# Kernel tuning notes

Measured on AMD Instinct MI355X. Metric: run time of the kernel, lower is better.

Reference implementation:

```python
import jax, jax.numpy as jnp
import numpy as np

CHUNK = (10, 10, 10)          # chunk_shape from init_kwargs
VSHAPE = (40, 40, 200)        # spatial shape of each block
GRID_MAX = 1000               # locations drawn from [0, GRID_MAX)
SPAN = 256                    # > (GRID_MAX + max(VSHAPE)) / min(CHUNK); per-dim chunk-grid span for key linearization
NBATCH = 64


def setup_inputs() -> dict:
    key = jax.random.key(0)
    k1, k2 = jax.random.split(key)
    data = jax.random.normal(k1, (NBATCH, *VSHAPE), dtype=jnp.float32)
    location = jax.random.randint(k2, (NBATCH, 3), 0, GRID_MAX, dtype=jnp.int32)
    return {"data": data, "location": location}


def _chunkify(data, location):
    """Rebin each block into chunk-grid-aligned tiles of shape CHUNK.
    data: [B, V0, V1, V2]; location: [B, 3] int offsets in the global grid.
    Returns (chunks [M, *CHUNK], locs [M, 3]) with M = B * prod(nchunks)."""
    B = data.shape[0]
    C = jnp.array(CHUNK, dtype=jnp.int32)
    shift = location % C          # [B,3] offset of block origin within its first chunk
    start = location - shift      # [B,3] chunk-aligned envelope origin
    # Fixed-size envelope V + C per dim covers any shift in [0, C).
    E = tuple(v + c for v, c in zip(VSHAPE, CHUNK))
    nch = tuple(e // c for e, c in zip(E, CHUNK))  # chunks per dim: (5, 5, 21)

    def pad_one(d, sh):
        # padded[j0,j1,j2] = d[j - sh] where in range, else 0 (gather + mask, no scatter)
        idx = [jnp.arange(E[k]) - sh[k] for k in range(3)]
        valid = [(ix >= 0) & (ix < VSHAPE[k]) for k, ix in enumerate(idx)]
        cidx = [jnp.clip(ix, 0, VSHAPE[k] - 1) for k, ix in enumerate(idx)]
        g = d[cidx[0][:, None, None], cidx[1][None, :, None], cidx[2][None, None, :]]
        m = valid[0][:, None, None] & valid[1][None, :, None] & valid[2][None, None, :]
        return jnp.where(m, g, jnp.float32(0))

    padded = jax.vmap(pad_one)(data, shift)  # [B, E0, E1, E2]
    padded = padded.reshape(B, nch[0], CHUNK[0], nch[1], CHUNK[1], nch[2], CHUNK[2])
    chunks = padded.transpose(0, 1, 3, 5, 2, 4, 6).reshape(-1, *CHUNK)
    # per-chunk global locations
    g = jnp.stack(jnp.meshgrid(jnp.arange(nch[0]), jnp.arange(nch[1]),
                               jnp.arange(nch[2]), indexing='ij'), axis=-1)  # [n0,n1,n2,3]
    locs = start[:, None, None, None, :] + g[None].astype(jnp.int32) * C     # [B,n0,n1,n2,3]
    return chunks, locs.reshape(-1, 3)


def _accumulate(chunks, locs):
    """Sum chunks sharing the same global chunk location (scatter-add reduce).
    Output padded to a fixed M rows (jit-friendly); padding rows are zero."""
    M = chunks.shape[0]
    C = jnp.array(CHUNK, dtype=jnp.int32)
    cg = locs // C  # chunk-grid coordinates, each < SPAN
    keys = (cg[:, 0] * SPAN + cg[:, 1]) * SPAN + cg[:, 2]  # int32 linearized key
    ukeys, inv = jnp.unique(keys, return_inverse=True, size=M,
                            fill_value=jnp.int32(2**31 - 1))
    out = jax.ops.segment_sum(chunks.reshape(M, -1), inv, num_segments=M)
    out = out.reshape(M, *CHUNK)
    uloc = jnp.stack([ukeys // (SPAN * SPAN), (ukeys // SPAN) % SPAN,
                      ukeys % SPAN], axis=-1).astype(jnp.int32) * C
    return out, uloc


def reference(data, location):
    chunks, locs = _chunkify(data, location)
    return _accumulate(chunks, locs)
```

## Files before the change

### kernel.cpp

```cpp
#include <hip/hip_runtime.h>
#include <hip/hip_bf16.h>

namespace {
constexpr int NB    = 64;
constexpr int V0d   = 40, V1d = 40, V2d = 200;
constexpr int VOL   = V0d * V1d * V2d;
constexpr int NC0   = 5, NC1 = 5, NC2 = 21;
constexpr int CELLS = NC0 * NC1 * NC2;
constexpr int M     = NB * CELLS;
constexpr int C1MAX = 104, C2MAX = 120;
constexpr int KS    = 104 * C1MAX * C2MAX;
constexpr int SEG   = 4096;
constexpr int NSEG  = (KS + SEG - 1) / SEG;
constexpr int KSP   = NSEG * SEG;
constexpr int CHVOL = 1000;
}

__device__ __forceinline__ float bf16r(float v) {
    return __bfloat162float(__float2bfloat16(v));
}

__device__ __forceinline__ int enc(int c0, int c1, int c2) {
    return (c0 * C1MAX + c1) * C2MAX + c2;
}

__global__ void k_zero(int* __restrict__ P, int4* __restrict__ mask4) {
    int idx = blockIdx.x * blockDim.x + threadIdx.x;
    int stride = gridDim.x * blockDim.x;
    int4* p4 = reinterpret_cast<int4*>(P);
    const int n4 = KSP / 4;
    for (int i = idx; i < n4; i += stride) p4[i] = make_int4(0, 0, 0, 0);
    const int m4 = M * 8 / 16;
    for (int i = idx; i < m4; i += stride) mask4[i] = make_int4(0, 0, 0, 0);
}

__global__ void k_mark(const int* __restrict__ loc, int* __restrict__ P) {
    int m = blockIdx.x * blockDim.x + threadIdx.x;
    if (m >= M) return;
    int b = m / CELLS, cell = m % CELLS;
    int i = cell / (NC1 * NC2), j = (cell / NC2) % NC1, k = cell % NC2;
    P[enc(loc[b * 3 + 0] / 10 + i, loc[b * 3 + 1] / 10 + j,
          loc[b * 3 + 2] / 10 + k)] = 1;
}

__global__ __launch_bounds__(256) void k_scan_blocks(int* __restrict__ P,
                                                     int* __restrict__ Bsums) {
    int bid = blockIdx.x, t = threadIdx.x;
    int4* p4 = reinterpret_cast<int4*>(P + (size_t)bid * SEG + t * 16);
    int4 a = p4[0], b = p4[1], c = p4[2], d = p4[3];
    int v[16] = {a.x, a.y, a.z, a.w, b.x, b.y, b.z, b.w,
                 c.x, c.y, c.z, c.w, d.x, d.y, d.z, d.w};
    int s = 0;
#pragma unroll
    for (int e = 0; e < 16; ++e) s += v[e];
    __shared__ int sc[256];
    sc[t] = s;
    __syncthreads();
#pragma unroll
    for (int off = 1; off < 256; off <<= 1) {
        int x = (t >= off) ? sc[t - off] : 0;
        __syncthreads();
        sc[t] += x;
        __syncthreads();
    }
    int incl = sc[t];
    if (t == 255) Bsums[bid] = incl;
    int run = incl - s;
#pragma unroll
    for (int e = 0; e < 16; ++e) { int x = v[e]; v[e] = run; run += x; }
    p4[0] = make_int4(v[0], v[1], v[2], v[3]);
    p4[1] = make_int4(v[4], v[5], v[6], v[7]);
    p4[2] = make_int4(v[8], v[9], v[10], v[11]);
    p4[3] = make_int4(v[12], v[13], v[14], v[15]);
}

__global__ __launch_bounds__(256) void k_scan_sums(int* __restrict__ Bsums,
                                                   int* __restrict__ U) {
    __shared__ int sc[256];
    __shared__ int carry_s;
    int t = threadIdx.x;
    if (t == 0) carry_s = 0;
    __syncthreads();
    for (int base = 0; base < NSEG; base += 256) {
        int idx = base + t;
        int vv = (idx < NSEG) ? Bsums[idx] : 0;
        sc[t] = vv;
        __syncthreads();
#pragma unroll
        for (int off = 1; off < 256; off <<= 1) {
            int x = (t >= off) ? sc[t - off] : 0;
            __syncthreads();
            sc[t] += x;
            __syncthreads();
        }
        int incl = sc[t];
        int carry = carry_s;
        if (idx < NSEG) Bsums[idx] = carry + incl - vv;
        __syncthreads();
        if (t == 255) carry_s = carry + incl;
        __syncthreads();
    }
    if (t == 0) U[0] = carry_s;
}

__global__ void k_slots(const int* __restrict__ loc, const int* __restrict__ P,
                        const int* __restrict__ Bsums, int* __restrict__ ukeys,
                        unsigned long long* __restrict__ mask) {
    int m = blockIdx.x * blockDim.x + threadIdx.x;
    if (m >= M) return;
    int b = m / CELLS, cell = m % CELLS;
    int i = cell / (NC1 * NC2), j = (cell / NC2) % NC1, k = cell % NC2;
    int d = enc(loc[b * 3 + 0] / 10 + i, loc[b * 3 + 1] / 10 + j,
                loc[b * 3 + 2] / 10 + k);
    int rank = P[d] + Bsums[d / SEG];
    ukeys[rank] = d;
    atomicOr(&mask[rank], 1ull << b);
}

__global__ __launch_bounds__(256) void k_out(const float* __restrict__ data,
                                             const int* __restrict__ loc,
                                             const int* __restrict__ ukeys,
                                             const unsigned long long* __restrict__ mask,
                                             const int* __restrict__ U,
                                             float* __restrict__ out,
                                             long long base_ul) {
    int orig = blockIdx.x;
    int r = (orig & 7) * (M / 8) + (orig >> 3);
    int t = threadIdx.x;

    __shared__ int sloc[NB * 3];
    __shared__ int skey, sU;
    __shared__ unsigned long long smask;
    if (t < NB * 3) sloc[t] = loc[t];
    if (t == 0) {
        sU = U[0];
        skey = ukeys[r];
        smask = mask[r];
    }
    __syncthreads();

    bool valid = (r < sU);
    float acc[4] = {0.f, 0.f, 0.f, 0.f};
    int c0 = 0, c1 = 0, c2 = 0;
    if (valid) {
        int d = skey;
        c0 = d / (C1MAX * C2MAX);
        int rem = d % (C1MAX * C2MAX);
        c1 = rem / C2MAX;
        c2 = rem % C2MAX;
        int g0 = c0 * 10, g1 = c1 * 10, g2 = c2 * 10;
        int ex[4], ey[4], ez[4];
#pragma unroll
        for (int q = 0; q < 4; ++q) {
            int e = t + 256 * q;
            ex[q] = e / 100; ey[q] = (e / 10) % 10; ez[q] = e % 10;
        }
        unsigned long long mk = smask;
        while (mk) {
            int b = __builtin_ctzll(mk);
            mk &= mk - 1;
            int l0 = sloc[b * 3 + 0], l1 = sloc[b * 3 + 1], l2 = sloc[b * 3 + 2];
            const float* db = data + (size_t)b * VOL;
            int o0 = g0 - l0, o1 = g1 - l1, o2 = g2 - l2;
#pragma unroll
            for (int q = 0; q < 4; ++q) {
                int e = t + 256 * q;
                if (e < CHVOL) {
                    int p0 = o0 + ex[q], p1 = o1 + ey[q], p2 = o2 + ez[q];
                    if ((unsigned)p0 < (unsigned)V0d &&
                        (unsigned)p1 < (unsigned)V1d &&
                        (unsigned)p2 < (unsigned)V2d)
                        acc[q] += db[(p0 * V1d + p1) * V2d + p2];
                }
            }
        }
    }
#pragma unroll
    for (int q = 0; q < 4; ++q) {
        int e = t + 256 * q;
        if (e < CHVOL)
            out[(long long)r * CHVOL + e] = bf16r(acc[q]);
    }
    if (t == 0) {
        float u0, u1, u2;
        if (valid) {
            u0 = (float)(c0 * 10);
            u1 = (float)(c1 * 10);
            u2 = (float)(c2 * 10);
        } else {
            u0 = 327670.f; u1 = 2550.f; u2 = 2550.f;
        }
        long long i = base_ul + (long long)r * 3;
        out[i + 0] = bf16r(u0);
        out[i + 1] = bf16r(u1);
        out[i + 2] = bf16r(u2);
    }
}

extern "C" void kernel_launch(void* const* d_in, const int* in_sizes, int n_in,
                              void* d_out, int out_size, void* d_ws, size_t ws_size,
                              hipStream_t stream) {
    const float* data = (const float*)d_in[0];
    const int* loc    = (const int*)d_in[1];
    float* out        = (float*)d_out;

    const size_t bytesP  = (size_t)KSP * 4;
    const size_t bytesSm = (size_t)M * 8
                         + (size_t)(NSEG + 64) * 4
                         + (size_t)M * 4 + 64;
    char* ws = (char*)d_ws;
    int* P;
    char* smalls;
    if (ws_size >= bytesP + bytesSm) {
        P      = (int*)ws;
        smalls = ws + bytesP;
    } else {
        P      = (int*)d_out;
        smalls = ws;
    }
    unsigned long long* mask = (unsigned long long*)smalls;
    int* Bsums = (int*)(smalls + (size_t)M * 8);
    int* ukeys = Bsums + NSEG + 64;
    int* U     = ukeys + M;

    long long out_sz  = (long long)out_size;
    long long base_ul = out_sz - (long long)3 * M;

    k_zero<<<640, 256, 0, stream>>>(P, (int4*)mask);
    k_mark<<<(M + 255) / 256, 256, 0, stream>>>(loc, P);
    k_scan_blocks<<<NSEG, 256, 0, stream>>>(P, Bsums);
    k_scan_sums<<<1, 256, 0, stream>>>(Bsums, U);
    k_slots<<<(M + 255) / 256, 256, 0, stream>>>(loc, P, Bsums, ukeys, mask);
    k_out<<<M, 256, 0, stream>>>(data, loc, ukeys, mask, U, out, base_ul);
}
```

Baseline: 70.69 us.

## Process four output chunks per block with branchless prefetched gathers and float4 stores

The output kernel now handles four unique chunk rows per block instead of one. Each thread owns four contiguous elements, which allows float4 stores. The first contributing source block for every row is loaded up front with clamped, predicated gathers so the loads can be issued together, and the shared-memory staging and barrier are removed. The trade-offs are more registers, four times fewer blocks, and serial per-row loops over any remaining contributors.

```diff
diff --git a/kernel.cpp b/kernel.cpp
--- a/kernel.cpp
+++ b/kernel.cpp
@@ -14,6 +14,8 @@
 constexpr int NSEG  = (KS + SEG - 1) / SEG;
 constexpr int KSP   = NSEG * SEG;
 constexpr int CHVOL = 1000;
+constexpr int RPB   = 4;
+constexpr int NQ    = M / RPB;
 }
 
 __device__ __forceinline__ float bf16r(float v) {
@@ -125,72 +127,104 @@
                                              float* __restrict__ out,
                                              long long base_ul) {
     int orig = blockIdx.x;
-    int r = (orig & 7) * (M / 8) + (orig >> 3);
+    int q = (orig & 7) * (NQ / 8) + (orig >> 3);
+    int r0 = q * RPB;
     int t = threadIdx.x;
-
-    __shared__ int sloc[NB * 3];
-    __shared__ int skey, sU;
-    __shared__ unsigned long long smask;
-    if (t < NB * 3) sloc[t] = loc[t];
-    if (t == 0) {
-        sU = U[0];
-        skey = ukeys[r];
-        smask = mask[r];
-    }
-    __syncthreads();
-
-    bool valid = (r < sU);
-    float acc[4] = {0.f, 0.f, 0.f, 0.f};
-    int c0 = 0, c1 = 0, c2 = 0;
-    if (valid) {
-        int d = skey;
-        c0 = d / (C1MAX * C2MAX);
+    int U0 = U[0];
+
+    int e0 = t * 4;
+    int xj[4], yj[4], zj[4];
+#pragma unroll
+    for (int j = 0; j < 4; ++j) {
+        int e = e0 + j;
+        xj[j] = e / 100; yj[j] = (e / 10) % 10; zj[j] = e % 10;
+    }
+
+    float acc[RPB][4] = {};
+    unsigned long long mk2[RPB];
+    int c0v[RPB], c1v[RPB], c2v[RPB];
+    bool vR[RPB];
+
+#pragma unroll
+    for (int rk = 0; rk < RPB; ++rk) {
+        int r = r0 + rk;
+        bool valid = (r < U0);
+        vR[rk] = valid;
+        int d = valid ? ukeys[r] : 0;
+        unsigned long long mk = valid ? mask[r] : 0ull;
+        int c0 = d / (C1MAX * C2MAX);
         int rem = d % (C1MAX * C2MAX);
-        c1 = rem / C2MAX;
-        c2 = rem % C2MAX;
-        int g0 = c0 * 10, g1 = c1 * 10, g2 = c2 * 10;
-        int ex[4], ey[4], ez[4];
-#pragma unroll
-        for (int q = 0; q < 4; ++q) {
-            int e = t + 256 * q;
-            ex[q] = e / 100; ey[q] = (e / 10) % 10; ez[q] = e % 10;
-        }
-        unsigned long long mk = smask;
+        int c1 = rem / C2MAX, c2 = rem % C2MAX;
+        c0v[rk] = c0; c1v[rk] = c1; c2v[rk] = c2;
+        bool any = (mk != 0ull);
+        int b = any ? __builtin_ctzll(mk) : 0;
+        mk2[rk] = any ? (mk & (mk - 1)) : 0ull;
+        int l0 = loc[b * 3 + 0], l1 = loc[b * 3 + 1], l2 = loc[b * 3 + 2];
+        int o0 = any ? (c0 * 10 - l0) : -1000;
+        int o1 = c1 * 10 - l1, o2 = c2 * 10 - l2;
+        const float* db = data + (size_t)b * VOL;
+#pragma unroll
+        for (int j = 0; j < 4; ++j) {
+            int p0 = o0 + xj[j], p1 = o1 + yj[j], p2 = o2 + zj[j];
+            bool v = ((unsigned)p0 < (unsigned)V0d) &
+                     ((unsigned)p1 < (unsigned)V1d) &
+                     ((unsigned)p2 < (unsigned)V2d);
+            int lin = (p0 * V1d + p1) * V2d + p2;
+            lin = lin < 0 ? 0 : (lin > VOL - 1 ? VOL - 1 : lin);
+            float val = db[lin];
+            acc[rk][j] += v ? val : 0.f;
+        }
+    }
+
+#pragma unroll
+    for (int rk = 0; rk < RPB; ++rk) {
+        unsigned long long mk = mk2[rk];
         while (mk) {
             int b = __builtin_ctzll(mk);
             mk &= mk - 1;
-            int l0 = sloc[b * 3 + 0], l1 = sloc[b * 3 + 1], l2 = sloc[b * 3 + 2];
+            int l0 = loc[b * 3 + 0], l1 = loc[b * 3 + 1], l2 = loc[b * 3 + 2];
+            int o0 = c0v[rk] * 10 - l0, o1 = c1v[rk] * 10 - l1,
+                o2 = c2v[rk] * 10 - l2;
             const float* db = data + (size_t)b * VOL;
-            int o0 = g0 - l0, o1 = g1 - l1, o2 = g2 - l2;
-#pragma unroll
-            for (int q = 0; q < 4; ++q) {
-                int e = t + 256 * q;
-                if (e < CHVOL) {
-                    int p0 = o0 + ex[q], p1 = o1 + ey[q], p2 = o2 + ez[q];
-                    if ((unsigned)p0 < (unsigned)V0d &&
-                        (unsigned)p1 < (unsigned)V1d &&
-                        (unsigned)p2 < (unsigned)V2d)
-                        acc[q] += db[(p0 * V1d + p1) * V2d + p2];
-                }
+#pragma unroll
+            for (int j = 0; j < 4; ++j) {
+                int p0 = o0 + xj[j], p1 = o1 + yj[j], p2 = o2 + zj[j];
+                bool v = ((unsigned)p0 < (unsigned)V0d) &
+                         ((unsigned)p1 < (unsigned)V1d) &
+                         ((unsigned)p2 < (unsigned)V2d);
+                int lin = (p0 * V1d + p1) * V2d + p2;
+                lin = lin < 0 ? 0 : (lin > VOL - 1 ? VOL - 1 : lin);
+                float val = db[lin];
+                acc[rk][j] += v ? val : 0.f;
             }
         }
     }
-#pragma unroll
-    for (int q = 0; q < 4; ++q) {
-        int e = t + 256 * q;
-        if (e < CHVOL)
-            out[(long long)r * CHVOL + e] = bf16r(acc[q]);
-    }
-    if (t == 0) {
+
+    if (t < 250) {
+#pragma unroll
+        for (int rk = 0; rk < RPB; ++rk) {
+            *reinterpret_cast<float4*>(out + (long long)(r0 + rk) * CHVOL + e0) =
+                make_float4(bf16r(acc[rk][0]), bf16r(acc[rk][1]),
+                            bf16r(acc[rk][2]), bf16r(acc[rk][3]));
+        }
+    }
+
+    if (t < RPB) {
+        bool v;
+        int c0, c1, c2;
+        if (t == 0)      { v = vR[0]; c0 = c0v[0]; c1 = c1v[0]; c2 = c2v[0]; }
+        else if (t == 1) { v = vR[1]; c0 = c0v[1]; c1 = c1v[1]; c2 = c2v[1]; }
+        else if (t == 2) { v = vR[2]; c0 = c0v[2]; c1 = c1v[2]; c2 = c2v[2]; }
+        else             { v = vR[3]; c0 = c0v[3]; c1 = c1v[3]; c2 = c2v[3]; }
         float u0, u1, u2;
-        if (valid) {
+        if (v) {
             u0 = (float)(c0 * 10);
             u1 = (float)(c1 * 10);
             u2 = (float)(c2 * 10);
         } else {
             u0 = 327670.f; u1 = 2550.f; u2 = 2550.f;
         }
-        long long i = base_ul + (long long)r * 3;
+        long long i = base_ul + (long long)(r0 + t) * 3;
         out[i + 0] = bf16r(u0);
         out[i + 1] = bf16r(u1);
         out[i + 2] = bf16r(u2);
@@ -231,5 +265,5 @@
     k_scan_blocks<<<NSEG, 256, 0, stream>>>(P, Bsums);
     k_scan_sums<<<1, 256, 0, stream>>>(Bsums, U);
     k_slots<<<(M + 255) / 256, 256, 0, stream>>>(loc, P, Bsums, ukeys, mask);
-    k_out<<<M, 256, 0, stream>>>(data, loc, ukeys, mask, U, out, base_ul);
-}
+    k_out<<<NQ, 256, 0, stream>>>(data, loc, ukeys, mask, U, out, base_ul);
+}
```

After: 70.50 us. About the same (-0.3%).
